# Performance work log

Measured on AMD Instinct MI355X. Metric: run time of the kernel, lower is better.

The kernel has to match this reference:

```python
import jax, jax.numpy as jnp
import numpy as np

NODE_DIM = 32
EDGE_DIM = 16
N_A = 1024
N_B = 1024
EDGE_IN = 2 * NODE_DIM + 2 * EDGE_DIM   # 96
NODE_IN = NODE_DIM + EDGE_DIM           # 48


def _linear_init(key, fan_in, fan_out):
    # torch nn.Linear default init: U(-1/sqrt(fan_in), 1/sqrt(fan_in))
    kw, kb = jax.random.split(key)
    bound = 1.0 / np.sqrt(fan_in)
    W = jax.random.uniform(kw, (fan_in, fan_out), jnp.float32, -bound, bound)
    b = jax.random.uniform(kb, (fan_out,), jnp.float32, -bound, bound)
    return W, b


def setup_inputs() -> dict:
    key = jax.random.key(0)
    ks = jax.random.split(key, 7)
    edge_embeds = jax.random.normal(ks[0], (N_A, N_B, 2 * EDGE_DIM), jnp.float32)
    nodes_a_embeds = jax.random.normal(ks[1], (N_A, NODE_DIM), jnp.float32)
    nodes_b_embeds = jax.random.normal(ks[2], (N_B, NODE_DIM), jnp.float32)
    We1, be1 = _linear_init(ks[3], EDGE_IN, EDGE_DIM)
    We2, be2 = _linear_init(ks[4], EDGE_DIM, EDGE_DIM)
    Wn1, bn1 = _linear_init(ks[5], NODE_IN, NODE_DIM)
    Wn2, bn2 = _linear_init(ks[6], NODE_DIM, NODE_DIM)
    return {
        "edge_embeds": edge_embeds,
        "nodes_a_embeds": nodes_a_embeds,
        "nodes_b_embeds": nodes_b_embeds,
        "We1": We1, "be1": be1, "We2": We2, "be2": be2,
        "Wn1": Wn1, "bn1": bn1, "Wn2": Wn2, "bn2": bn2,
    }


def _edge_mlp(x, We1, be1, We2, be2):
    h = jax.nn.relu(x @ We1 + be1)
    return jax.nn.relu(h @ We2 + be2)


def _node_mlp(x, Wn1, bn1, Wn2, bn2):
    h = jax.nn.relu(x @ Wn1 + bn1)
    return jax.nn.relu(h @ Wn2 + bn2)


def reference(edge_embeds, nodes_a_embeds, nodes_b_embeds,
              We1, be1, We2, be2, Wn1, bn1, Wn2, bn2):
    nA, nB, _ = edge_embeds.shape
    # edge update: broadcast node feats over the bipartite grid, concat, 2-layer MLP
    a_bcast = jnp.broadcast_to(nodes_a_embeds[:, None, :], (nA, nB, NODE_DIM))
    b_bcast = jnp.broadcast_to(nodes_b_embeds[None, :, :], (nA, nB, NODE_DIM))
    edge_in = jnp.concatenate([a_bcast, b_bcast, edge_embeds], axis=-1)  # (A,B,96)
    new_edges = _edge_mlp(edge_in, We1, be1, We2, be2)                   # (A,B,E)
    # node update: sum-aggregate messages, concat with node feats, 2-layer MLP
    msg_to_a = new_edges.sum(axis=1)  # (A,E)
    msg_to_b = new_edges.sum(axis=0)  # (B,E)
    new_a = _node_mlp(jnp.concatenate([nodes_a_embeds, msg_to_a], axis=-1), Wn1, bn1, Wn2, bn2)
    new_b = _node_mlp(jnp.concatenate([nodes_b_embeds, msg_to_b], axis=-1), Wn1, bn1, Wn2, bn2)
    return (new_edges, new_a, new_b)
```

## Files before the change

kernel.cpp:

```cpp
#include <hip/hip_runtime.h>
#include <hip/hip_bf16.h>

typedef float f32x4 __attribute__((ext_vector_type(4)));
typedef short s16x8 __attribute__((ext_vector_type(8)));
typedef short s16x4 __attribute__((ext_vector_type(4)));

__device__ __forceinline__ unsigned short f2bf(float x) {
  return __bfloat16_as_ushort(__float2bfloat16(x));
}

__device__ __forceinline__ f32x4 mfma16x16x16_bf16(s16x4 a, s16x4 b, f32x4 c) {
#if __has_builtin(__builtin_amdgcn_mfma_f32_16x16x16bf16_1k)
  return __builtin_amdgcn_mfma_f32_16x16x16bf16_1k(a, b, c, 0, 0, 0);
#else
  f32x4 d;
  asm("v_mfma_f32_16x16x16_bf16 %0, %1, %2, %3" : "=v"(d) : "v"(a), "v"(b), "v"(c));
  return d;
#endif
}

__global__ __launch_bounds__(256, 4)
void edge_kernel(const float* __restrict__ E,
                 const float* __restrict__ na,
                 const float* __restrict__ nb,
                 const float* __restrict__ We1,
                 const float* __restrict__ be1,
                 const float* __restrict__ We2,
                 const float* __restrict__ be2,
                 float* __restrict__ outE,
                 float* __restrict__ rowP,
                 float* __restrict__ colP) {
  __shared__ float sA[32 * 16];
  __shared__ float sB[32 * 20];
  __shared__ float sCS[4 * 512];

  const int t = threadIdx.x;
  const int bi = blockIdx.y, bj = blockIdx.x;

  {
    const bool half = t >= 128;
    const int tt = t & 127, r = tt >> 2, qs = (tt & 3) << 2;
    const float* x = (half ? nb : na) + (half ? bj : bi) * 32 * 32 + r * 32;
    const float* W = We1 + (half ? 32 * 16 : 0) + qs;
    f32x4 acc;
    if (half) acc = *(const f32x4*)&be1[qs];
    else { acc[0] = acc[1] = acc[2] = acc[3] = 0.f; }
#pragma unroll 8
    for (int v = 0; v < 32; ++v) {
      float xv = x[v];
      f32x4 wv = *(const f32x4*)&W[v * 16];
      acc[0] += xv * wv[0]; acc[1] += xv * wv[1];
      acc[2] += xv * wv[2]; acc[3] += xv * wv[3];
    }
    if (half) *(f32x4*)&sB[r * 20 + qs] = acc;
    else      *(f32x4*)&sA[r * 16 + qs] = acc;
  }

  const int w = t >> 6, lane = t & 63, G = lane >> 4, n = lane & 15;

  s16x8 a1;
  s16x4 a2;
#pragma unroll
  for (int i2 = 0; i2 < 8; ++i2) a1[i2] = (short)f2bf(We1[(64 + G * 8 + i2) * 16 + n]);
#pragma unroll
  for (int i2 = 0; i2 < 4; ++i2) a2[i2] = (short)f2bf(We2[(G * 4 + i2) * 16 + n]);
  const f32x4 bq = *(const f32x4*)&be2[G * 4];

  __syncthreads();

  f32x4 cs0 = {0.f, 0.f, 0.f, 0.f}, cs1 = {0.f, 0.f, 0.f, 0.f};
  const f32x4 zero = {0.f, 0.f, 0.f, 0.f};
  const f32x4 pB0 = *(const f32x4*)&sB[n * 20 + G * 4];
  const f32x4 pB1 = *(const f32x4*)&sB[(16 + n) * 20 + G * 4];

#pragma unroll 2
  for (int ii = 0; ii < 8; ++ii) {
    const int iloc = w * 8 + ii;
    const int i = bi * 32 + iloc;
    const float* ep = E + ((long)(i * 1024 + bj * 32 + n) << 5) + G * 8;
    f32x4 e00 = __builtin_nontemporal_load((const f32x4*)ep);
    f32x4 e01 = __builtin_nontemporal_load((const f32x4*)(ep + 4));
    f32x4 e10 = __builtin_nontemporal_load((const f32x4*)(ep + 512));
    f32x4 e11 = __builtin_nontemporal_load((const f32x4*)(ep + 516));
    const f32x4 pA = *(const f32x4*)&sA[iloc * 16 + G * 4];
    f32x4 rs = {0.f, 0.f, 0.f, 0.f};
#pragma unroll
    for (int jg = 0; jg < 2; ++jg) {
      const f32x4 ea = jg ? e10 : e00;
      const f32x4 eb = jg ? e11 : e01;
      const f32x4 pB = jg ? pB1 : pB0;
      const int j = bj * 32 + jg * 16 + n;
      s16x8 bf;
      bf[0] = (short)f2bf(ea[0]); bf[1] = (short)f2bf(ea[1]);
      bf[2] = (short)f2bf(ea[2]); bf[3] = (short)f2bf(ea[3]);
      bf[4] = (short)f2bf(eb[0]); bf[5] = (short)f2bf(eb[1]);
      bf[6] = (short)f2bf(eb[2]); bf[7] = (short)f2bf(eb[3]);
      f32x4 d1 = __builtin_amdgcn_mfma_f32_16x16x32_bf16(a1, bf, zero, 0, 0, 0);
      float h0 = fmaxf(d1[0] + pA[0] + pB[0], 0.f);
      float h1 = fmaxf(d1[1] + pA[1] + pB[1], 0.f);
      float h2 = fmaxf(d1[2] + pA[2] + pB[2], 0.f);
      float h3 = fmaxf(d1[3] + pA[3] + pB[3], 0.f);
      s16x4 b2;
      b2[0] = (short)f2bf(h0); b2[1] = (short)f2bf(h1);
      b2[2] = (short)f2bf(h2); b2[3] = (short)f2bf(h3);
      f32x4 d2 = mfma16x16x16_bf16(a2, b2, zero);
      f32x4 o;
      o[0] = fmaxf(d2[0] + bq[0], 0.f);
      o[1] = fmaxf(d2[1] + bq[1], 0.f);
      o[2] = fmaxf(d2[2] + bq[2], 0.f);
      o[3] = fmaxf(d2[3] + bq[3], 0.f);
      __builtin_nontemporal_store(o, (f32x4*)&outE[((long)(i * 1024 + j) << 4) + G * 4]);
      rs += o;
      if (jg == 0) cs0 += o; else cs1 += o;
    }
#pragma unroll
    for (int mask = 1; mask < 16; mask <<= 1) {
      rs[0] += __shfl_xor(rs[0], mask);
      rs[1] += __shfl_xor(rs[1], mask);
      rs[2] += __shfl_xor(rs[2], mask);
      rs[3] += __shfl_xor(rs[3], mask);
    }
    if (n < 4) {
      float val = (n == 0) ? rs[0] : (n == 1) ? rs[1] : (n == 2) ? rs[2] : rs[3];
      rowP[bj * 16384 + i * 16 + G * 4 + n] = val;
    }
  }
  *(f32x4*)&sCS[w * 512 + n * 16 + G * 4] = cs0;
  *(f32x4*)&sCS[w * 512 + 256 + n * 16 + G * 4] = cs1;
  __syncthreads();
#pragma unroll
  for (int rep = 0; rep < 2; ++rep) {
    int idx = t + rep * 256;
    float s = sCS[idx] + sCS[512 + idx] + sCS[1024 + idx] + sCS[1536 + idx];
    int jl = idx >> 4, c = idx & 15;
    colP[bi * 16384 + (bj * 32 + jl) * 16 + c] = s;
  }
}

__global__ void node_kernel(const float* __restrict__ na, const float* __restrict__ nb,
                            const float* __restrict__ rowP, const float* __restrict__ colP,
                            const float* __restrict__ Wn1, const float* __restrict__ bn1,
                            const float* __restrict__ Wn2, const float* __restrict__ bn2,
                            float* __restrict__ outA, float* __restrict__ outB) {
  int tid = blockIdx.x * blockDim.x + threadIdx.x;
  bool isB = tid >= 1024;
  int row = tid & 1023;
  const float* x0 = (isB ? nb : na) + row * 32;
  const float* P = (isB ? colP : rowP) + row * 16;
  f32x4 m0 = {0.f,0.f,0.f,0.f}, m1 = m0, m2 = m0, m3 = m0;
#pragma unroll 4
  for (int b = 0; b < 32; ++b) {
    const float* p = P + b * 16384;
    m0 += *(const f32x4*)&p[0];
    m1 += *(const f32x4*)&p[4];
    m2 += *(const f32x4*)&p[8];
    m3 += *(const f32x4*)&p[12];
  }
  union { f32x4 v[4]; float f[16]; } mm;
  mm.v[0] = m0; mm.v[1] = m1; mm.v[2] = m2; mm.v[3] = m3;

  float h[32];
#pragma unroll
  for (int m = 0; m < 32; ++m) h[m] = bn1[m];
#pragma unroll 4
  for (int v = 0; v < 32; ++v) {
    float xv = x0[v];
#pragma unroll
    for (int m = 0; m < 32; ++m) h[m] += xv * Wn1[v * 32 + m];
  }
#pragma unroll 4
  for (int v = 0; v < 16; ++v) {
    float mv = mm.f[v];
#pragma unroll
    for (int m = 0; m < 32; ++m) h[m] += mv * Wn1[(32 + v) * 32 + m];
  }
#pragma unroll
  for (int m = 0; m < 32; ++m) h[m] = fmaxf(h[m], 0.f);
  float* dst = (isB ? outB : outA) + row * 32;
#pragma unroll 4
  for (int c = 0; c < 32; ++c) {
    float s = bn2[c];
#pragma unroll
    for (int m = 0; m < 32; ++m) s += h[m] * Wn2[m * 32 + c];
    dst[c] = fmaxf(s, 0.f);
  }
}

extern "C" void kernel_launch(void* const* d_in, const int* in_sizes, int n_in,
                              void* d_out, int out_size, void* d_ws, size_t ws_size,
                              hipStream_t stream) {
  const float* E   = (const float*)d_in[0];
  const float* na  = (const float*)d_in[1];
  const float* nb  = (const float*)d_in[2];
  const float* We1 = (const float*)d_in[3];
  const float* be1 = (const float*)d_in[4];
  const float* We2 = (const float*)d_in[5];
  const float* be2 = (const float*)d_in[6];
  const float* Wn1 = (const float*)d_in[7];
  const float* bn1 = (const float*)d_in[8];
  const float* Wn2 = (const float*)d_in[9];
  const float* bn2 = (const float*)d_in[10];

  float* out  = (float*)d_out;
  float* outE = out;
  float* outA = out + 16777216;
  float* outB = outA + 32768;

  float* ws   = (float*)d_ws;
  float* rowP = ws;
  float* colP = ws + 524288;

  edge_kernel<<<dim3(32, 32), dim3(256), 0, stream>>>(E, na, nb, We1, be1, We2, be2,
                                                      outE, rowP, colP);
  node_kernel<<<dim3(8), dim3(256), 0, stream>>>(na, nb, rowP, colP,
                                                 Wn1, bn1, Wn2, bn2, outA, outB);
}
```

Measured before the change: 258.0 us.

## Parallelize node MLP across 128 blocks with per-output-column threads

Replaces the 8-block node kernel, where each thread handled one node and kept a 32-wide hidden vector in registers, with a 128-block kernel. Each block reduces the partial messages for 16 nodes, staging them in shared memory, and then computes the two MLP layers with one thread per (node, output column). The aim is to cut the latency of the serial tail kernel by spreading the work over many more CUs and making the partial-sum loads coalesced. The cost is extra shared-memory traffic and two block-wide barriers per block.

```diff
diff --git a/kernel.cpp b/kernel.cpp
--- a/kernel.cpp
+++ b/kernel.cpp
@@ -137,52 +137,54 @@
   }
 }
 
-__global__ void node_kernel(const float* __restrict__ na, const float* __restrict__ nb,
-                            const float* __restrict__ rowP, const float* __restrict__ colP,
-                            const float* __restrict__ Wn1, const float* __restrict__ bn1,
-                            const float* __restrict__ Wn2, const float* __restrict__ bn2,
-                            float* __restrict__ outA, float* __restrict__ outB) {
-  int tid = blockIdx.x * blockDim.x + threadIdx.x;
-  bool isB = tid >= 1024;
-  int row = tid & 1023;
-  const float* x0 = (isB ? nb : na) + row * 32;
-  const float* P = (isB ? colP : rowP) + row * 16;
-  f32x4 m0 = {0.f,0.f,0.f,0.f}, m1 = m0, m2 = m0, m3 = m0;
-#pragma unroll 4
-  for (int b = 0; b < 32; ++b) {
-    const float* p = P + b * 16384;
-    m0 += *(const f32x4*)&p[0];
-    m1 += *(const f32x4*)&p[4];
-    m2 += *(const f32x4*)&p[8];
-    m3 += *(const f32x4*)&p[12];
-  }
-  union { f32x4 v[4]; float f[16]; } mm;
-  mm.v[0] = m0; mm.v[1] = m1; mm.v[2] = m2; mm.v[3] = m3;
-
-  float h[32];
-#pragma unroll
-  for (int m = 0; m < 32; ++m) h[m] = bn1[m];
-#pragma unroll 4
-  for (int v = 0; v < 32; ++v) {
-    float xv = x0[v];
-#pragma unroll
-    for (int m = 0; m < 32; ++m) h[m] += xv * Wn1[v * 32 + m];
-  }
-#pragma unroll 4
-  for (int v = 0; v < 16; ++v) {
-    float mv = mm.f[v];
-#pragma unroll
-    for (int m = 0; m < 32; ++m) h[m] += mv * Wn1[(32 + v) * 32 + m];
-  }
-#pragma unroll
-  for (int m = 0; m < 32; ++m) h[m] = fmaxf(h[m], 0.f);
-  float* dst = (isB ? outB : outA) + row * 32;
-#pragma unroll 4
-  for (int c = 0; c < 32; ++c) {
-    float s = bn2[c];
-#pragma unroll
-    for (int m = 0; m < 32; ++m) s += h[m] * Wn2[m * 32 + c];
-    dst[c] = fmaxf(s, 0.f);
+__global__ __launch_bounds__(256)
+void reduce_node_kernel(const float* __restrict__ na, const float* __restrict__ nb,
+                        const float* __restrict__ rowP, const float* __restrict__ colP,
+                        const float* __restrict__ Wn1, const float* __restrict__ bn1,
+                        const float* __restrict__ Wn2, const float* __restrict__ bn2,
+                        float* __restrict__ outA, float* __restrict__ outB) {
+  __shared__ float smsg[16 * 16];
+  __shared__ float sh[16 * 33];
+
+  const int b = blockIdx.x;
+  const bool isB = b >= 64;
+  const int r0 = (b & 63) * 16;
+  const int t = threadIdx.x;
+
+  {
+    const float* P = isB ? colP : rowP;
+    int off = r0 * 16 + t;
+    float s = 0.f;
+#pragma unroll 8
+    for (int sl = 0; sl < 32; ++sl) s += P[sl * 16384 + off];
+    smsg[t] = s;
+  }
+  __syncthreads();
+
+  const float* x0base = (isB ? nb : na) + r0 * 32;
+  const int m = t & 31, rl = t >> 5;
+
+#pragma unroll
+  for (int pass = 0; pass < 2; ++pass) {
+    const int row = rl + pass * 8;
+    const float* x0 = x0base + row * 32;
+    float s = bn1[m];
+#pragma unroll 8
+    for (int v = 0; v < 32; ++v) s += x0[v] * Wn1[v * 32 + m];
+#pragma unroll 8
+    for (int v = 0; v < 16; ++v) s += smsg[row * 16 + v] * Wn1[(32 + v) * 32 + m];
+    sh[row * 33 + m] = fmaxf(s, 0.f);
+  }
+  __syncthreads();
+
+  float* dst = (isB ? outB : outA);
+#pragma unroll
+  for (int pass = 0; pass < 2; ++pass) {
+    const int row = rl + pass * 8;
+    float s = bn2[m];
+#pragma unroll 8
+    for (int mm = 0; mm < 32; ++mm) s += sh[row * 33 + mm] * Wn2[mm * 32 + m];
+    dst[(r0 + row) * 32 + m] = fmaxf(s, 0.f);
   }
 }
 
@@ -212,6 +214,6 @@
 
   edge_kernel<<<dim3(32, 32), dim3(256), 0, stream>>>(E, na, nb, We1, be1, We2, be2,
                                                       outE, rowP, colP);
-  node_kernel<<<dim3(8), dim3(256), 0, stream>>>(na, nb, rowP, colP,
-                                                 Wn1, bn1, Wn2, bn2, outA, outB);
-}
+  reduce_node_kernel<<<dim3(128), dim3(256), 0, stream>>>(na, nb, rowP, colP,
+                                                          Wn1, bn1, Wn2, bn2, outA, outB);
+}
```

After: 239.9 us. 7.0% less time.
